# Kernel tuning notes

Hardware: AMD Instinct MI355X
Metric: run time of the kernel (lower is better)

The kernel has to match this reference:

```python
import jax, jax.numpy as jnp
import numpy as np

B, T, C, H = 4, 2048, 1024, 16
DK = C // H


def setup_inputs() -> dict:
    key = jax.random.key(0)
    ks = jax.random.split(key, 12)
    s = 1.0 / np.sqrt(C)
    return {
        "q": jax.random.normal(ks[0], (B, T, C), jnp.float32),
        "k": jax.random.normal(ks[1], (B, T, C), jnp.float32),
        "v": jax.random.normal(ks[2], (B, T, C), jnp.float32),
        "mask": jax.random.randint(ks[3], (B, T, T), 0, 2, jnp.int32),
        "Wq": jax.random.normal(ks[4], (C, C), jnp.float32) * s,
        "bq": jnp.zeros((C,), jnp.float32),
        "Wk": jax.random.normal(ks[5], (C, C), jnp.float32) * s,
        "bk": jnp.zeros((C,), jnp.float32),
        "Wv": jax.random.normal(ks[6], (C, C), jnp.float32) * s,
        "bv": jnp.zeros((C,), jnp.float32),
        "Wf": jax.random.normal(ks[7], (C, C), jnp.float32) * s,
        "bf": jnp.zeros((C,), jnp.float32),
    }


def reference(q, k, v, mask, Wq, bq, Wk, bk, Wv, bv, Wf, bf):
    # linear projections (torch Linear: x @ W.T + b), then split heads
    def heads(x, W, b):
        y = x @ W.T + b  # [B,T,C]
        return y.reshape(B, T, H, DK).transpose(0, 2, 1, 3)  # [B,H,T,DK]

    qh, kh, vh = heads(q, Wq, bq), heads(k, Wk, bk), heads(v, Wv, bv)
    att = jnp.einsum("bhqd,bhkd->bhqk", qh, kh) * (1.0 / np.sqrt(DK))
    att = jnp.where(mask[:, None, :, :] == 0, jnp.float32(-1e9), att)
    p = jax.nn.softmax(att, axis=-1)
    y = jnp.einsum("bhqk,bhkd->bhqd", p, vh)  # [B,H,T,DK]
    y = y.transpose(0, 2, 1, 3).reshape(B, T, C)
    return y @ Wf.T + bf
```

## Files before the change

### kernel.cpp

```cpp
#include <hip/hip_runtime.h>

#define B_ 4
#define T_ 2048
#define C_ 1024
#define H_ 16
#define DK_ 64
#define BT_ 8192

using u16 = unsigned short;
using u32 = unsigned int;
using u64 = unsigned long long;
typedef __attribute__((ext_vector_type(8))) short short8;
typedef __attribute__((ext_vector_type(4))) float f32x4;
typedef __attribute__((ext_vector_type(16))) float f32x16;
typedef __attribute__((ext_vector_type(4))) u32 u32x4;
typedef __attribute__((ext_vector_type(2))) u32 u32x2;

__device__ __forceinline__ u16 f2bf(float f) {
  u32 u = __builtin_bit_cast(u32, f);
  u32 r = u + 0x7fffu + ((u >> 16) & 1u);
  return (u16)(r >> 16);
}

__device__ __forceinline__ void glds16(void* lds, const void* g) {
  __builtin_amdgcn_global_load_lds(
      (__attribute__((address_space(1))) u32*)g,
      (__attribute__((address_space(3))) u32*)lds, 16, 0, 0);
}

__device__ __forceinline__ u32 cvtpk_bf16(float lo, float hi) {
  u32 r;
  asm("v_cvt_pk_bf16_f32 %0, %1, %2" : "=v"(r) : "v"(lo), "v"(hi));
  return r;
}

__device__ __forceinline__ void cvt_range(const float* __restrict__ s,
                                          u16* __restrict__ d, int n,
                                          int rb, int nblk) {
  int i0 = (rb * 256 + (int)threadIdx.x) * 4;
  int stride = nblk * 256 * 4;
  for (int i = i0; i < n; i += stride) {
    float4 v = *(const float4*)(s + i);
    u64 p = (u64)f2bf(v.x) | ((u64)f2bf(v.y) << 16) |
            ((u64)f2bf(v.z) << 32) | ((u64)f2bf(v.w) << 48);
    *(u64*)(d + i) = p;
  }
}

__global__ __launch_bounds__(256) void prep_k(
    const float* __restrict__ q, const float* __restrict__ k,
    const float* __restrict__ v, const float* __restrict__ Wq,
    const float* __restrict__ Wk, const float* __restrict__ Wv,
    const float* __restrict__ Wf,
    u16* __restrict__ qb, u16* __restrict__ kb, u16* __restrict__ vb,
    u16* __restrict__ Wqb, u16* __restrict__ Wkb, u16* __restrict__ Wvb,
    u16* __restrict__ Wfb) {
  const int bid = blockIdx.x;
  if (bid < 1890) {
    const int which = bid / 630, rb = bid % 630;
    const float* s = which == 0 ? q : which == 1 ? k : v;
    u16* d = which == 0 ? qb : which == 1 ? kb : vb;
    cvt_range(s, d, BT_ * C_, rb, 630);
  } else if (bid < 2046) {
    const int idx = bid - 1890;
    const int which = idx / 39, rb = idx % 39;
    const float* s = which == 0 ? Wq : which == 1 ? Wk : which == 2 ? Wv : Wf;
    u16* d = which == 0 ? Wqb : which == 1 ? Wkb : which == 2 ? Wvb : Wfb;
    cvt_range(s, d, C_ * C_, rb, 39);
  }
}

__global__ __launch_bounds__(256) void proj_k(
    const u16* __restrict__ qb, const u16* __restrict__ kb,
    const u16* __restrict__ vb,
    const u16* __restrict__ Wqb, const u16* __restrict__ Wkb,
    const u16* __restrict__ Wvb,
    const float* __restrict__ bq, const float* __restrict__ bk,
    const float* __restrict__ bv,
    u16* __restrict__ Qh, u16* __restrict__ Kh, u16* __restrict__ Vt,
    const int* __restrict__ mask, u64* __restrict__ mb, float qscale) {
  __shared__ __align__(16) u16 As[128 * 32];
  __shared__ __align__(16) u16 Bs[128 * 32];
  const int z = blockIdx.z;
  const int t = threadIdx.x;

  if (z == 3) {
    const int fid = blockIdx.y * 64 + blockIdx.x;
    const int lane = t & 63;
    const int nch = B_ * T_ * T_ / 256;
    int g0 = fid * 16 + (t >> 6) * 4;
    for (int g = g0; g < nch; g += 512 * 16) {
#pragma unroll
      for (int gg = 0; gg < 4; ++gg) {
        const int4 vv = *(const int4*)(mask + (size_t)(g + gg) * 256 + 4 * lane);
        const u64 b0 = __ballot(vv.x != 0);
        const u64 b1 = __ballot(vv.y != 0);
        const u64 b2 = __ballot(vv.z != 0);
        const u64 b3 = __ballot(vv.w != 0);
        const u64 wv = lane == 0 ? b0 : lane == 1 ? b1 : lane == 2 ? b2 : b3;
        if (lane < 4) mb[(size_t)(g + gg) * 4 + lane] = wv;
      }
    }
    return;
  }

  const u16* A = z == 0 ? qb : z == 1 ? kb : Wvb;
  const u16* Bm = z == 0 ? Wqb : z == 1 ? Wkb : vb;
  const float* bias = z == 0 ? bq : z == 1 ? bk : bv;
  u16* out = z == 0 ? Qh : z == 1 ? Kh : Vt;
  const float scale = z == 0 ? qscale : 1.0f;
  const int m0 = (z == 2 ? blockIdx.y : blockIdx.x) * 128;
  const int n0 = (z == 2 ? blockIdx.x : blockIdx.y) * 128;
  const int N = z == 2 ? BT_ : C_;
  const int K = C_;

  const int lane = t & 63;
  const int wave = t >> 6;
  const int wr = wave >> 1, wc = wave & 1;
  const int lr = lane & 15, lg = lane >> 4;

  f32x4 acc[4][4] = {};

  const int srow = t >> 2;
  const int scol = (t & 3) * 8;
  const u16* ag = A + (size_t)(m0 + srow) * K + scol;
  const u16* bg = Bm + (size_t)(n0 + srow) * K + scol;
  u16* as0 = &As[srow * 32 + scol];
  u16* as1 = &As[(srow + 64) * 32 + scol];
  u16* bs0 = &Bs[srow * 32 + scol];
  u16* bs1 = &Bs[(srow + 64) * 32 + scol];

  for (int k0 = 0; k0 < K; k0 += 32) {
    glds16(as0, ag + k0);
    glds16(as1, ag + (size_t)64 * K + k0);
    glds16(bs0, bg + k0);
    glds16(bs1, bg + (size_t)64 * K + k0);
    __syncthreads();
    short8 af[4], bf[4];
#pragma unroll
    for (int m = 0; m < 4; ++m)
      af[m] = *(const short8*)&As[(wr * 64 + m * 16 + lr) * 32 + lg * 8];
#pragma unroll
    for (int n = 0; n < 4; ++n)
      bf[n] = *(const short8*)&Bs[(wc * 64 + n * 16 + lr) * 32 + lg * 8];
#pragma unroll
    for (int m = 0; m < 4; ++m)
#pragma unroll
      for (int n = 0; n < 4; ++n)
        acc[m][n] = __builtin_amdgcn_mfma_f32_16x16x32_bf16(af[m], bf[n], acc[m][n], 0, 0, 0);
    __syncthreads();
  }

#pragma unroll
  for (int m = 0; m < 4; ++m) {
#pragma unroll
    for (int n = 0; n < 4; ++n) {
#pragma unroll
      for (int j = 0; j < 4; ++j) {
        const int gm = m0 + wr * 64 + m * 16 + lg * 4 + j;
        const int gn = n0 + wc * 64 + n * 16 + lr;
        float v = acc[m][n][j];
        if (z <= 1) {
          v = (v + bias[gn]) * scale;
          const int b = gm >> 11, tt = gm & 2047, h = gn >> 6, d = gn & 63;
          out[((((size_t)b * H_ + h) * T_ + tt) << 6) + d] = f2bf(v);
        } else {
          v += bias[gm];
          const int gnp = (gn & ~12) | ((gn & 4) << 1) | ((gn & 8) >> 1);
          out[(size_t)gm * N + gnp] = f2bf(v);
        }
      }
    }
  }
}

__global__ __launch_bounds__(256) void out_k(
    const u16* __restrict__ A, const u16* __restrict__ Bm,
    const float* __restrict__ bias, float* __restrict__ out,
    int M, int N, int K) {
  __shared__ __align__(16) u16 As[128 * 32];
  __shared__ __align__(16) u16 Bs[128 * 32];
  const int t = threadIdx.x;
  const int lane = t & 63;
  const int wave = t >> 6;
  const int wr = wave >> 1, wc = wave & 1;
  const int lr = lane & 15, lg = lane >> 4;
  const int m0 = blockIdx.x * 128;
  const int n0 = blockIdx.y * 128;

  f32x4 acc[4][4] = {};

  const int srow = t >> 2;
  const int scol = (t & 3) * 8;
  const u16* ag = A + (size_t)(m0 + srow) * K + scol;
  const u16* bg = Bm + (size_t)(n0 + srow) * K + scol;
  u16* as0 = &As[srow * 32 + scol];
  u16* as1 = &As[(srow + 64) * 32 + scol];
  u16* bs0 = &Bs[srow * 32 + scol];
  u16* bs1 = &Bs[(srow + 64) * 32 + scol];

  for (int k0 = 0; k0 < K; k0 += 32) {
    glds16(as0, ag + k0);
    glds16(as1, ag + (size_t)64 * K + k0);
    glds16(bs0, bg + k0);
    glds16(bs1, bg + (size_t)64 * K + k0);
    __syncthreads();
    short8 af[4], bf[4];
#pragma unroll
    for (int m = 0; m < 4; ++m)
      af[m] = *(const short8*)&As[(wr * 64 + m * 16 + lr) * 32 + lg * 8];
#pragma unroll
    for (int n = 0; n < 4; ++n)
      bf[n] = *(const short8*)&Bs[(wc * 64 + n * 16 + lr) * 32 + lg * 8];
#pragma unroll
    for (int m = 0; m < 4; ++m)
#pragma unroll
      for (int n = 0; n < 4; ++n)
        acc[m][n] = __builtin_amdgcn_mfma_f32_16x16x32_bf16(af[m], bf[n], acc[m][n], 0, 0, 0);
    __syncthreads();
  }

#pragma unroll
  for (int m = 0; m < 4; ++m)
#pragma unroll
    for (int n = 0; n < 4; ++n)
#pragma unroll
      for (int j = 0; j < 4; ++j) {
        const int gm = m0 + wr * 64 + m * 16 + lg * 4 + j;
        const int gn = n0 + wc * 64 + n * 16 + lr;
        out[(size_t)gm * N + gn] = acc[m][n][j] + bias[gn];
      }
}

__global__ __launch_bounds__(512) void attn32_k(
    const u16* __restrict__ Qh, const u16* __restrict__ Kh,
    const u16* __restrict__ Vt, const u64* __restrict__ mb,
    u16* __restrict__ Y) {
  __shared__ __align__(16) u16 Ks[2][128 * 68];
  __shared__ __align__(16) u16 Vs[2][64 * 132];

  const int f = blockIdx.x;
  const int lgid = ((f & 7) << 6) | (f >> 3);
  const int bh = lgid >> 3, qblk = lgid & 7;
  const int b = bh >> 4, h = bh & 15;
  const int t = threadIdx.x;
  const int wave = t >> 6, lane = t & 63;
  const int lq = lane & 31, hi = lane >> 5;
  const int q0 = qblk * 256 + wave * 32;

  const u16* Qp = Qh + ((size_t)bh * T_ + q0 + lq) * DK_ + hi * 8;
  short8 qf[4];
#pragma unroll
  for (int kt = 0; kt < 4; ++kt) qf[kt] = *(const short8*)(Qp + kt * 16);

  const u16* KgB = Kh + (size_t)bh * T_ * DK_;
  const u16* VtB = Vt + (size_t)h * DK_ * BT_ + (size_t)b * T_;
  const u64* mrow = mb + ((size_t)b * T_ + q0 + lq) * (T_ / 64);

  const int kr = t >> 3, ku = t & 7;
  const u16* ksrcA = KgB + (size_t)kr * DK_ + ku * 8;
  const u16* ksrcB = KgB + (size_t)(kr + 64) * DK_ + ku * 8;
  const int kdstA = kr * 68 + ku * 8, kdstB = (kr + 64) * 68 + ku * 8;
  const int vr = t >> 4, vu = t & 15;
  const u16* vsrcA = VtB + (size_t)vr * BT_ + vu * 8;
  const u16* vsrcB = VtB + (size_t)(vr + 32) * BT_ + vu * 8;
  const int vdstA = vr * 132 + vu * 8, vdstB = (vr + 32) * 132 + vu * 8;

  const u32x4 onesu = {0x3F803F80u, 0x3F803F80u, 0x3F803F80u, 0x3F803F80u};
  const short8 ones8 = __builtin_bit_cast(short8, onesu);

  f32x16 o0 = {}, o1 = {}, accl = {};

  u32x4 kpA = *(const u32x4*)(ksrcA), kpB = *(const u32x4*)(ksrcB);
  u32x4 vpA = *(const u32x4*)(vsrcA), vpB = *(const u32x4*)(vsrcB);
  *(u32x2*)&Ks[0][kdstA] = (u32x2){kpA[0], kpA[1]};
  *(u32x2*)&Ks[0][kdstA + 4] = (u32x2){kpA[2], kpA[3]};
  *(u32x2*)&Ks[0][kdstB] = (u32x2){kpB[0], kpB[1]};
  *(u32x2*)&Ks[0][kdstB + 4] = (u32x2){kpB[2], kpB[3]};
  *(u32x2*)&Vs[0][vdstA] = (u32x2){vpA[0], vpA[1]};
  *(u32x2*)&Vs[0][vdstA + 4] = (u32x2){vpA[2], vpA[3]};
  *(u32x2*)&Vs[0][vdstB] = (u32x2){vpB[0], vpB[1]};
  *(u32x2*)&Vs[0][vdstB + 4] = (u32x2){vpB[2], vpB[3]};
  __syncthreads();
  int cur = 0;

  for (int kv = 0; kv < T_; kv += 128) {
    const bool pre = (kv + 128) < T_;
    if (pre) {
      kpA = *(const u32x4*)(ksrcA + (size_t)(kv + 128) * DK_);
      kpB = *(const u32x4*)(ksrcB + (size_t)(kv + 128) * DK_);
      vpA = *(const u32x4*)(vsrcA + (kv + 128));
      vpB = *(const u32x4*)(vsrcB + (kv + 128));
    }

#pragma unroll
    for (int s2 = 0; s2 < 2; ++s2) {
      const int kvs = kv + 64 * s2;
      f32x16 c0 = {}, c1 = {};
      __builtin_amdgcn_s_setprio(1);
#pragma unroll
      for (int kt = 0; kt < 4; ++kt) {
        const int ix = (2 * kt + hi) * 8;
        const u32x2 a0 = *(const u32x2*)&Ks[cur][(64 * s2 + lq) * 68 + ix];
        const u32x2 a1 = *(const u32x2*)&Ks[cur][(64 * s2 + lq) * 68 + ix + 4];
        const u32x2 b0 = *(const u32x2*)&Ks[cur][(64 * s2 + lq + 32) * 68 + ix];
        const u32x2 b1 = *(const u32x2*)&Ks[cur][(64 * s2 + lq + 32) * 68 + ix + 4];
        const u32x4 k0u = {a0[0], a0[1], a1[0], a1[1]};
        const u32x4 k1u = {b0[0], b0[1], b1[0], b1[1]};
        c0 = __builtin_amdgcn_mfma_f32_32x32x16_bf16(
            __builtin_bit_cast(short8, k0u), qf[kt], c0, 0, 0, 0);
        c1 = __builtin_amdgcn_mfma_f32_32x32x16_bf16(
            __builtin_bit_cast(short8, k1u), qf[kt], c1, 0, 0, 0);
      }
      __builtin_amdgcn_s_setprio(0);

      const u64* wp = mrow + ((kvs >> 8) << 2);
      const int sh = ((kvs >> 2) & 48) + hi;
      u32 tp[4];
#pragma unroll
      for (int e = 0; e < 4; ++e) tp[e] = (u32)(wp[e] >> sh);
#pragma unroll
      for (int r = 0; r < 16; ++r) {
        const int pp = 2 * (r >> 2);
        const u32 k0m = (u32)(((int)(tp[r & 3] << (31 - pp))) >> 31);
        const u32 k1m = (u32)(((int)(tp[r & 3] << (23 - pp))) >> 31);
        c0[r] = __builtin_bit_cast(
            float, __builtin_bit_cast(u32, __builtin_amdgcn_exp2f(c0[r])) & k0m);
        c1[r] = __builtin_bit_cast(
            float, __builtin_bit_cast(u32, __builtin_amdgcn_exp2f(c1[r])) & k1m);
      }

      u32 pw_[4][4];
#pragma unroll
      for (int g = 0; g < 4; ++g) {
        const int ob = (g & 1) * 8;
#pragma unroll
        for (int w2 = 0; w2 < 4; ++w2) {
          const float lo = (g < 2) ? c0[ob + 2 * w2] : c1[ob + 2 * w2];
          const float hii = (g < 2) ? c0[ob + 2 * w2 + 1] : c1[ob + 2 * w2 + 1];
          pw_[g][w2] = cvtpk_bf16(lo, hii);
        }
      }

      __builtin_amdgcn_s_setprio(1);
#pragma unroll
      for (int g = 0; g < 4; ++g) {
        const int ix = 16 * (4 * s2 + g) + 8 * hi;
        const u32x2 va = *(const u32x2*)&Vs[cur][lq * 132 + ix];
        const u32x2 vb = *(const u32x2*)&Vs[cur][lq * 132 + ix + 4];
        const u32x2 wa = *(const u32x2*)&Vs[cur][(lq + 32) * 132 + ix];
        const u32x2 wb = *(const u32x2*)&Vs[cur][(lq + 32) * 132 + ix + 4];
        const u32x4 pu = {pw_[g][0], pw_[g][1], pw_[g][2], pw_[g][3]};
        const u32x4 v0u = {va[0], va[1], vb[0], vb[1]};
        const u32x4 v1u = {wa[0], wa[1], wb[0], wb[1]};
        const short8 pa = __builtin_bit_cast(short8, pu);
        o0 = __builtin_amdgcn_mfma_f32_32x32x16_bf16(
            pa, __builtin_bit_cast(short8, v0u), o0, 0, 0, 0);
        o1 = __builtin_amdgcn_mfma_f32_32x32x16_bf16(
            pa, __builtin_bit_cast(short8, v1u), o1, 0, 0, 0);
        accl = __builtin_amdgcn_mfma_f32_32x32x16_bf16(pa, ones8, accl, 0, 0, 0);
      }
      __builtin_amdgcn_s_setprio(0);
    }

    if (pre) {
      *(u32x2*)&Ks[cur ^ 1][kdstA] = (u32x2){kpA[0], kpA[1]};
      *(u32x2*)&Ks[cur ^ 1][kdstA + 4] = (u32x2){kpA[2], kpA[3]};
      *(u32x2*)&Ks[cur ^ 1][kdstB] = (u32x2){kpB[0], kpB[1]};
      *(u32x2*)&Ks[cur ^ 1][kdstB + 4] = (u32x2){kpB[2], kpB[3]};
      *(u32x2*)&Vs[cur ^ 1][vdstA] = (u32x2){vpA[0], vpA[1]};
      *(u32x2*)&Vs[cur ^ 1][vdstA + 4] = (u32x2){vpA[2], vpA[3]};
      *(u32x2*)&Vs[cur ^ 1][vdstB] = (u32x2){vpB[0], vpB[1]};
      *(u32x2*)&Vs[cur ^ 1][vdstB + 4] = (u32x2){vpB[2], vpB[3]};
    }
    __syncthreads();
    cur ^= 1;
  }

#pragma unroll
  for (int r = 0; r < 16; ++r) {
    const int row = (r & 3) + 8 * (r >> 2) + 4 * hi;
    const float li = 1.0f / accl[r];
    u16* yp = Y + ((size_t)b * T_ + q0 + row) * C_ + h * DK_ + lq;
    yp[0] = f2bf(o0[r] * li);
    yp[32] = f2bf(o1[r] * li);
  }
}

extern "C" void kernel_launch(void* const* d_in, const int* in_sizes, int n_in,
                              void* d_out, int out_size, void* d_ws, size_t ws_size,
                              hipStream_t stream) {
  const float* q  = (const float*)d_in[0];
  const float* k  = (const float*)d_in[1];
  const float* v  = (const float*)d_in[2];
  const int* mask = (const int*)d_in[3];
  const float* Wq = (const float*)d_in[4];
  const float* bq = (const float*)d_in[5];
  const float* Wk = (const float*)d_in[6];
  const float* bk = (const float*)d_in[7];
  const float* Wv = (const float*)d_in[8];
  const float* bv = (const float*)d_in[9];
  const float* Wf = (const float*)d_in[10];
  const float* bf = (const float*)d_in[11];
  float* out = (float*)d_out;
  char* ws = (char*)d_ws;

  size_t off = 0;
  auto nxt = [&](size_t bytes) -> void* {
    void* p = ws + off;
    off += (bytes + 255) & ~(size_t)255;
    return p;
  };
  const size_t big = (size_t)BT_ * C_ * 2;
  const size_t wsz = (size_t)C_ * C_ * 2;
  u16* qb  = (u16*)nxt(big);
  u16* kb  = (u16*)nxt(big);
  u16* vb  = (u16*)nxt(big);
  u16* Wqb = (u16*)nxt(wsz);
  u16* Wkb = (u16*)nxt(wsz);
  u16* Wvb = (u16*)nxt(wsz);
  u16* Wfb = (u16*)nxt(wsz);
  u16* Qh  = (u16*)nxt(big);
  u16* Kh  = (u16*)nxt(big);
  u16* Vt  = (u16*)nxt(big);
  u16* Yb  = (u16*)nxt(big);
  u64* mb  = (u64*)nxt((size_t)B_ * T_ * (T_ / 64) * 8);

  prep_k<<<2048, 256, 0, stream>>>(q, k, v, Wq, Wk, Wv, Wf,
                                   qb, kb, vb, Wqb, Wkb, Wvb, Wfb);

  const float qscale = 0.125f * 1.4426950408889634f;
  proj_k<<<dim3(64, 8, 4), 256, 0, stream>>>(
      qb, kb, vb, Wqb, Wkb, Wvb, bq, bk, bv, Qh, Kh, Vt, mask, mb, qscale);

  attn32_k<<<B_ * H_ * (T_ / 256), 512, 0, stream>>>(Qh, Kh, Vt, mb, Yb);

  out_k<<<dim3(BT_ / 128, C_ / 128), 256, 0, stream>>>(
      Yb, Wfb, bf, out, BT_, C_, C_);
}
```

Before: 270.5 us.

## Fuse fp32-to-bf16 activation conversion into projection GEMM tile loads

Removes the separate conversion pass for q, k and v. The projection kernel now loads fp32 activation tiles straight into XOR-swizzled LDS and converts them to bf16 when building the MFMA fragments. This avoids writing and re-reading three bf16 copies of the activations, at the cost of doubling LDS tile size and re-reading fp32 tiles across the column blocks. The prep kernel now converts only the weight matrices.

```diff
diff --git a/kernel.cpp b/kernel.cpp
--- a/kernel.cpp
+++ b/kernel.cpp
@@ -48,39 +48,28 @@
 }
 
 __global__ __launch_bounds__(256) void prep_k(
-    const float* __restrict__ q, const float* __restrict__ k,
-    const float* __restrict__ v, const float* __restrict__ Wq,
-    const float* __restrict__ Wk, const float* __restrict__ Wv,
-    const float* __restrict__ Wf,
-    u16* __restrict__ qb, u16* __restrict__ kb, u16* __restrict__ vb,
+    const float* __restrict__ Wq, const float* __restrict__ Wk,
+    const float* __restrict__ Wv, const float* __restrict__ Wf,
     u16* __restrict__ Wqb, u16* __restrict__ Wkb, u16* __restrict__ Wvb,
     u16* __restrict__ Wfb) {
   const int bid = blockIdx.x;
-  if (bid < 1890) {
-    const int which = bid / 630, rb = bid % 630;
-    const float* s = which == 0 ? q : which == 1 ? k : v;
-    u16* d = which == 0 ? qb : which == 1 ? kb : vb;
-    cvt_range(s, d, BT_ * C_, rb, 630);
-  } else if (bid < 2046) {
-    const int idx = bid - 1890;
-    const int which = idx / 39, rb = idx % 39;
-    const float* s = which == 0 ? Wq : which == 1 ? Wk : which == 2 ? Wv : Wf;
-    u16* d = which == 0 ? Wqb : which == 1 ? Wkb : which == 2 ? Wvb : Wfb;
-    cvt_range(s, d, C_ * C_, rb, 39);
-  }
+  const int which = bid >> 7, rb = bid & 127;
+  const float* s = which == 0 ? Wq : which == 1 ? Wk : which == 2 ? Wv : Wf;
+  u16* d = which == 0 ? Wqb : which == 1 ? Wkb : which == 2 ? Wvb : Wfb;
+  cvt_range(s, d, C_ * C_, rb, 128);
 }
 
 __global__ __launch_bounds__(256) void proj_k(
-    const u16* __restrict__ qb, const u16* __restrict__ kb,
-    const u16* __restrict__ vb,
+    const float* __restrict__ qf, const float* __restrict__ kf,
+    const float* __restrict__ vf,
     const u16* __restrict__ Wqb, const u16* __restrict__ Wkb,
     const u16* __restrict__ Wvb,
     const float* __restrict__ bq, const float* __restrict__ bk,
     const float* __restrict__ bv,
     u16* __restrict__ Qh, u16* __restrict__ Kh, u16* __restrict__ Vt,
     const int* __restrict__ mask, u64* __restrict__ mb, float qscale) {
-  __shared__ __align__(16) u16 As[128 * 32];
-  __shared__ __align__(16) u16 Bs[128 * 32];
+  __shared__ __align__(16) u16 As[128 * 64];
+  __shared__ __align__(16) u16 Bs[128 * 64];
   const int z = blockIdx.z;
   const int t = threadIdx.x;
 
@@ -104,8 +93,11 @@
     return;
   }
 
-  const u16* A = z == 0 ? qb : z == 1 ? kb : Wvb;
-  const u16* Bm = z == 0 ? Wqb : z == 1 ? Wkb : vb;
+  const bool afp = (z <= 1);
+  const float* Af = z == 0 ? qf : kf;
+  const u16* Ab = Wvb;
+  const u16* Bb = z == 0 ? Wqb : Wkb;
+  const float* Bf = vf;
   const float* bias = z == 0 ? bq : z == 1 ? bk : bv;
   u16* out = z == 0 ? Qh : z == 1 ? Kh : Vt;
   const float scale = z == 0 ? qscale : 1.0f;
@@ -123,26 +115,62 @@
 
   const int srow = t >> 2;
   const int scol = (t & 3) * 8;
-  const u16* ag = A + (size_t)(m0 + srow) * K + scol;
-  const u16* bg = Bm + (size_t)(n0 + srow) * K + scol;
-  u16* as0 = &As[srow * 32 + scol];
-  u16* as1 = &As[(srow + 64) * 32 + scol];
-  u16* bs0 = &Bs[srow * 32 + scol];
-  u16* bs1 = &Bs[(srow + 64) * 32 + scol];
+  float* Asf = (float*)As;
+  float* Bsf = (float*)Bs;
 
   for (int k0 = 0; k0 < K; k0 += 32) {
-    glds16(as0, ag + k0);
-    glds16(as1, ag + (size_t)64 * K + k0);
-    glds16(bs0, bg + k0);
-    glds16(bs1, bg + (size_t)64 * K + k0);
+    if (afp) {
+#pragma unroll
+      for (int s = 0; s < 4; ++s) {
+        const int c = t + s * 256;
+        const int row = c >> 3, cc = c & 7;
+        glds16(&As[row * 64 + cc * 8],
+               Af + (size_t)(m0 + row) * K + k0 + ((cc ^ (row & 7)) << 2));
+      }
+      glds16(&Bs[srow * 32 + scol], Bb + (size_t)(n0 + srow) * K + k0 + scol);
+      glds16(&Bs[(srow + 64) * 32 + scol],
+             Bb + (size_t)(n0 + srow + 64) * K + k0 + scol);
+    } else {
+      glds16(&As[srow * 32 + scol], Ab + (size_t)(m0 + srow) * K + k0 + scol);
+      glds16(&As[(srow + 64) * 32 + scol],
+             Ab + (size_t)(m0 + srow + 64) * K + k0 + scol);
+#pragma unroll
+      for (int s = 0; s < 4; ++s) {
+        const int c = t + s * 256;
+        const int row = c >> 3, cc = c & 7;
+        glds16(&Bs[row * 64 + cc * 8],
+               Bf + (size_t)(n0 + row) * K + k0 + ((cc ^ (row & 7)) << 2));
+      }
+    }
     __syncthreads();
     short8 af[4], bf[4];
-#pragma unroll
-    for (int m = 0; m < 4; ++m)
-      af[m] = *(const short8*)&As[(wr * 64 + m * 16 + lr) * 32 + lg * 8];
-#pragma unroll
-    for (int n = 0; n < 4; ++n)
-      bf[n] = *(const short8*)&Bs[(wc * 64 + n * 16 + lr) * 32 + lg * 8];
+    if (afp) {
+#pragma unroll
+      for (int m = 0; m < 4; ++m) {
+        const int row = wr * 64 + m * 16 + lr;
+        const f32x4 u0 = *(const f32x4*)&Asf[row * 32 + (((2 * lg) ^ (row & 7)) << 2)];
+        const f32x4 u1 = *(const f32x4*)&Asf[row * 32 + (((2 * lg + 1) ^ (row & 7)) << 2)];
+        const u32x4 p = {cvtpk_bf16(u0[0], u0[1]), cvtpk_bf16(u0[2], u0[3]),
+                         cvtpk_bf16(u1[0], u1[1]), cvtpk_bf16(u1[2], u1[3])};
+        af[m] = __builtin_bit_cast(short8, p);
+      }
+#pragma unroll
+      for (int n = 0; n < 4; ++n)
+        bf[n] = *(const short8*)&Bs[(wc * 64 + n * 16 + lr) * 32 + lg * 8];
+    } else {
+#pragma unroll
+      for (int m = 0; m < 4; ++m)
+        af[m] = *(const short8*)&As[(wr * 64 + m * 16 + lr) * 32 + lg * 8];
+#pragma unroll
+      for (int n = 0; n < 4; ++n) {
+        const int row = wc * 64 + n * 16 + lr;
+        const f32x4 u0 = *(const f32x4*)&Bsf[row * 32 + (((2 * lg) ^ (row & 7)) << 2)];
+        const f32x4 u1 = *(const f32x4*)&Bsf[row * 32 + (((2 * lg + 1) ^ (row & 7)) << 2)];
+        const u32x4 p = {cvtpk_bf16(u0[0], u0[1]), cvtpk_bf16(u0[2], u0[3]),
+                         cvtpk_bf16(u1[0], u1[1]), cvtpk_bf16(u1[2], u1[3])};
+        bf[n] = __builtin_bit_cast(short8, p);
+      }
+    }
 #pragma unroll
     for (int m = 0; m < 4; ++m)
 #pragma unroll
@@ -413,9 +441,6 @@
   };
   const size_t big = (size_t)BT_ * C_ * 2;
   const size_t wsz = (size_t)C_ * C_ * 2;
-  u16* qb  = (u16*)nxt(big);
-  u16* kb  = (u16*)nxt(big);
-  u16* vb  = (u16*)nxt(big);
   u16* Wqb = (u16*)nxt(wsz);
   u16* Wkb = (u16*)nxt(wsz);
   u16* Wvb = (u16*)nxt(wsz);
@@ -426,12 +451,11 @@
   u16* Yb  = (u16*)nxt(big);
   u64* mb  = (u64*)nxt((size_t)B_ * T_ * (T_ / 64) * 8);
 
-  prep_k<<<2048, 256, 0, stream>>>(q, k, v, Wq, Wk, Wv, Wf,
-                                   qb, kb, vb, Wqb, Wkb, Wvb, Wfb);
+  prep_k<<<512, 256, 0, stream>>>(Wq, Wk, Wv, Wf, Wqb, Wkb, Wvb, Wfb);
 
   const float qscale = 0.125f * 1.4426950408889634f;
   proj_k<<<dim3(64, 8, 4), 256, 0, stream>>>(
-      qb, kb, vb, Wqb, Wkb, Wvb, bq, bk, bv, Qh, Kh, Vt, mask, mb, qscale);
+      q, k, v, Wqb, Wkb, Wvb, bq, bk, bv, Qh, Kh, Vt, mask, mb, qscale);
 
   attn32_k<<<B_ * H_ * (T_ / 256), 512, 0, stream>>>(Qh, Kh, Vt, mb, Yb);
 
```

After: 300.1 us. 1.11x slower.

## Give each attention wave 64 query rows and compute softmax denominators with VALU sums

Applied to the files above, without the earlier changes.

The attention kernel now runs 4 waves per block instead of 8, and each wave handles 64 query rows as two 32-row sets. Every K and V fragment read from LDS therefore feeds twice as many MFMAs, which halves LDS traffic per unit of work. The row-sum MFMA against a ones vector is replaced by VALU accumulation of the probabilities, then a cross-lane shuffle reduction before normalisation. The cost is much higher register pressure (four score and four output accumulators per wave), which may lower occupancy or cause spills, and each thread now issues more global loads for the K/V tiles.

```diff
diff --git a/kernel.cpp b/kernel.cpp
--- a/kernel.cpp
+++ b/kernel.cpp
@@ -232,7 +232,7 @@
       }
 }
 
-__global__ __launch_bounds__(512) void attn32_k(
+__global__ __launch_bounds__(256) void attn64_k(
     const u16* __restrict__ Qh, const u16* __restrict__ Kh,
     const u16* __restrict__ Vt, const u64* __restrict__ mb,
     u16* __restrict__ Y) {
@@ -246,57 +246,93 @@
   const int t = threadIdx.x;
   const int wave = t >> 6, lane = t & 63;
   const int lq = lane & 31, hi = lane >> 5;
-  const int q0 = qblk * 256 + wave * 32;
-
-  const u16* Qp = Qh + ((size_t)bh * T_ + q0 + lq) * DK_ + hi * 8;
-  short8 qf[4];
-#pragma unroll
-  for (int kt = 0; kt < 4; ++kt) qf[kt] = *(const short8*)(Qp + kt * 16);
+  const int q0 = qblk * 256 + wave * 64;
+
+  short8 qf0[4], qf1[4];
+  {
+    const u16* Qp0 = Qh + ((size_t)bh * T_ + q0 + lq) * DK_ + hi * 8;
+    const u16* Qp1 = Qp0 + (size_t)32 * DK_;
+#pragma unroll
+    for (int kt = 0; kt < 4; ++kt) {
+      qf0[kt] = *(const short8*)(Qp0 + kt * 16);
+      qf1[kt] = *(const short8*)(Qp1 + kt * 16);
+    }
+  }
 
   const u16* KgB = Kh + (size_t)bh * T_ * DK_;
   const u16* VtB = Vt + (size_t)h * DK_ * BT_ + (size_t)b * T_;
-  const u64* mrow = mb + ((size_t)b * T_ + q0 + lq) * (T_ / 64);
-
-  const int kr = t >> 3, ku = t & 7;
-  const u16* ksrcA = KgB + (size_t)kr * DK_ + ku * 8;
-  const u16* ksrcB = KgB + (size_t)(kr + 64) * DK_ + ku * 8;
-  const int kdstA = kr * 68 + ku * 8, kdstB = (kr + 64) * 68 + ku * 8;
-  const int vr = t >> 4, vu = t & 15;
-  const u16* vsrcA = VtB + (size_t)vr * BT_ + vu * 8;
-  const u16* vsrcB = VtB + (size_t)(vr + 32) * BT_ + vu * 8;
-  const int vdstA = vr * 132 + vu * 8, vdstB = (vr + 32) * 132 + vu * 8;
-
-  const u32x4 onesu = {0x3F803F80u, 0x3F803F80u, 0x3F803F80u, 0x3F803F80u};
-  const short8 ones8 = __builtin_bit_cast(short8, onesu);
-
-  f32x16 o0 = {}, o1 = {}, accl = {};
-
-  u32x4 kpA = *(const u32x4*)(ksrcA), kpB = *(const u32x4*)(ksrcB);
-  u32x4 vpA = *(const u32x4*)(vsrcA), vpB = *(const u32x4*)(vsrcB);
-  *(u32x2*)&Ks[0][kdstA] = (u32x2){kpA[0], kpA[1]};
-  *(u32x2*)&Ks[0][kdstA + 4] = (u32x2){kpA[2], kpA[3]};
-  *(u32x2*)&Ks[0][kdstB] = (u32x2){kpB[0], kpB[1]};
-  *(u32x2*)&Ks[0][kdstB + 4] = (u32x2){kpB[2], kpB[3]};
-  *(u32x2*)&Vs[0][vdstA] = (u32x2){vpA[0], vpA[1]};
-  *(u32x2*)&Vs[0][vdstA + 4] = (u32x2){vpA[2], vpA[3]};
-  *(u32x2*)&Vs[0][vdstB] = (u32x2){vpB[0], vpB[1]};
-  *(u32x2*)&Vs[0][vdstB + 4] = (u32x2){vpB[2], vpB[3]};
+  const u64* mrow0 = mb + ((size_t)b * T_ + q0 + lq) * (T_ / 64);
+  const u64* mrow1 = mrow0 + (size_t)32 * (T_ / 64);
+
+  f32x16 o00 = {}, o01 = {}, o10 = {}, o11 = {};
+  float ps0[4] = {0.f, 0.f, 0.f, 0.f}, ps1[4] = {0.f, 0.f, 0.f, 0.f};
+
+  u32x4 kp[4], vp[4];
+#pragma unroll
+  for (int s = 0; s < 4; ++s) {
+    const int c = t + s * 256;
+    kp[s] = *(const u32x4*)(KgB + (size_t)(c >> 3) * DK_ + (c & 7) * 8);
+    vp[s] = *(const u32x4*)(VtB + (size_t)(c >> 4) * BT_ + (c & 15) * 8);
+  }
+#pragma unroll
+  for (int s = 0; s < 4; ++s) {
+    const int c = t + s * 256;
+    const int kd = (c >> 3) * 68 + (c & 7) * 8;
+    const int vd = (c >> 4) * 132 + (c & 15) * 8;
+    *(u32x2*)&Ks[0][kd] = (u32x2){kp[s][0], kp[s][1]};
+    *(u32x2*)&Ks[0][kd + 4] = (u32x2){kp[s][2], kp[s][3]};
+    *(u32x2*)&Vs[0][vd] = (u32x2){vp[s][0], vp[s][1]};
+    *(u32x2*)&Vs[0][vd + 4] = (u32x2){vp[s][2], vp[s][3]};
+  }
   __syncthreads();
   int cur = 0;
+
+  auto finish_set = [&](f32x16& ca, f32x16& cb, const u64* mrow,
+                        float (&ps)[4], u32 (&pw)[4][4], int kvs) {
+    const u64* wp = mrow + ((kvs >> 8) << 2);
+    const int sh = ((kvs >> 2) & 48) + hi;
+    u32 tp[4];
+#pragma unroll
+    for (int e = 0; e < 4; ++e) tp[e] = (u32)(wp[e] >> sh);
+#pragma unroll
+    for (int r = 0; r < 16; ++r) {
+      const int pp = 2 * (r >> 2);
+      const u32 k0m = (u32)(((int)(tp[r & 3] << (31 - pp))) >> 31);
+      const u32 k1m = (u32)(((int)(tp[r & 3] << (23 - pp))) >> 31);
+      ca[r] = __builtin_bit_cast(
+          float, __builtin_bit_cast(u32, __builtin_amdgcn_exp2f(ca[r])) & k0m);
+      cb[r] = __builtin_bit_cast(
+          float, __builtin_bit_cast(u32, __builtin_amdgcn_exp2f(cb[r])) & k1m);
+      ps[r & 3] += ca[r] + cb[r];
+    }
+#pragma unroll
+    for (int g = 0; g < 4; ++g) {
+      const int ob = (g & 1) * 8;
+#pragma unroll
+      for (int w2 = 0; w2 < 4; ++w2) {
+        const float lo = (g < 2) ? ca[ob + 2 * w2] : cb[ob + 2 * w2];
+        const float hii = (g < 2) ? ca[ob + 2 * w2 + 1] : cb[ob + 2 * w2 + 1];
+        pw[g][w2] = cvtpk_bf16(lo, hii);
+      }
+    }
+  };
 
   for (int kv = 0; kv < T_; kv += 128) {
     const bool pre = (kv + 128) < T_;
     if (pre) {
-      kpA = *(const u32x4*)(ksrcA + (size_t)(kv + 128) * DK_);
-      kpB = *(const u32x4*)(ksrcB + (size_t)(kv + 128) * DK_);
-      vpA = *(const u32x4*)(vsrcA + (kv + 128));
-      vpB = *(const u32x4*)(vsrcB + (kv + 128));
+#pragma unroll
+      for (int s = 0; s < 4; ++s) {
+        const int c = t + s * 256;
+        kp[s] = *(const u32x4*)(KgB + (size_t)(kv + 128 + (c >> 3)) * DK_ + (c & 7) * 8);
+        vp[s] = *(const u32x4*)(VtB + (size_t)(c >> 4) * BT_ + kv + 128 + (c & 15) * 8);
+      }
     }
 
 #pragma unroll
     for (int s2 = 0; s2 < 2; ++s2) {
       const int kvs = kv + 64 * s2;
-      f32x16 c0 = {}, c1 = {};
+
+      f32x16 c00 = {}, c01 = {}, c10 = {}, c11 = {};
       __builtin_amdgcn_s_setprio(1);
 #pragma unroll
       for (int kt = 0; kt < 4; ++kt) {
@@ -307,40 +343,18 @@
         const u32x2 b1 = *(const u32x2*)&Ks[cur][(64 * s2 + lq + 32) * 68 + ix + 4];
         const u32x4 k0u = {a0[0], a0[1], a1[0], a1[1]};
         const u32x4 k1u = {b0[0], b0[1], b1[0], b1[1]};
-        c0 = __builtin_amdgcn_mfma_f32_32x32x16_bf16(
-            __builtin_bit_cast(short8, k0u), qf[kt], c0, 0, 0, 0);
-        c1 = __builtin_amdgcn_mfma_f32_32x32x16_bf16(
-            __builtin_bit_cast(short8, k1u), qf[kt], c1, 0, 0, 0);
+        const short8 k0 = __builtin_bit_cast(short8, k0u);
+        const short8 k1 = __builtin_bit_cast(short8, k1u);
+        c00 = __builtin_amdgcn_mfma_f32_32x32x16_bf16(k0, qf0[kt], c00, 0, 0, 0);
+        c10 = __builtin_amdgcn_mfma_f32_32x32x16_bf16(k0, qf1[kt], c10, 0, 0, 0);
+        c01 = __builtin_amdgcn_mfma_f32_32x32x16_bf16(k1, qf0[kt], c01, 0, 0, 0);
+        c11 = __builtin_amdgcn_mfma_f32_32x32x16_bf16(k1, qf1[kt], c11, 0, 0, 0);
       }
       __builtin_amdgcn_s_setprio(0);
 
-      const u64* wp = mrow + ((kvs >> 8) << 2);
-      const int sh = ((kvs >> 2) & 48) + hi;
-      u32 tp[4];
-#pragma unroll
-      for (int e = 0; e < 4; ++e) tp[e] = (u32)(wp[e] >> sh);
-#pragma unroll
-      for (int r = 0; r < 16; ++r) {
-        const int pp = 2 * (r >> 2);
-        const u32 k0m = (u32)(((int)(tp[r & 3] << (31 - pp))) >> 31);
-        const u32 k1m = (u32)(((int)(tp[r & 3] << (23 - pp))) >> 31);
-        c0[r] = __builtin_bit_cast(
-            float, __builtin_bit_cast(u32, __builtin_amdgcn_exp2f(c0[r])) & k0m);
-        c1[r] = __builtin_bit_cast(
-            float, __builtin_bit_cast(u32, __builtin_amdgcn_exp2f(c1[r])) & k1m);
-      }
-
-      u32 pw_[4][4];
-#pragma unroll
-      for (int g = 0; g < 4; ++g) {
-        const int ob = (g & 1) * 8;
-#pragma unroll
-        for (int w2 = 0; w2 < 4; ++w2) {
-          const float lo = (g < 2) ? c0[ob + 2 * w2] : c1[ob + 2 * w2];
-          const float hii = (g < 2) ? c0[ob + 2 * w2 + 1] : c1[ob + 2 * w2 + 1];
-          pw_[g][w2] = cvtpk_bf16(lo, hii);
-        }
-      }
+      u32 pw0[4][4], pw1[4][4];
+      finish_set(c00, c01, mrow0, ps0, pw0, kvs);
+      finish_set(c10, c11, mrow1, ps1, pw1, kvs);
 
       __builtin_amdgcn_s_setprio(1);
 #pragma unroll
@@ -350,40 +364,54 @@
         const u32x2 vb = *(const u32x2*)&Vs[cur][lq * 132 + ix + 4];
         const u32x2 wa = *(const u32x2*)&Vs[cur][(lq + 32) * 132 + ix];
         const u32x2 wb = *(const u32x2*)&Vs[cur][(lq + 32) * 132 + ix + 4];
-        const u32x4 pu = {pw_[g][0], pw_[g][1], pw_[g][2], pw_[g][3]};
         const u32x4 v0u = {va[0], va[1], vb[0], vb[1]};
         const u32x4 v1u = {wa[0], wa[1], wb[0], wb[1]};
-        const short8 pa = __builtin_bit_cast(short8, pu);
-        o0 = __builtin_amdgcn_mfma_f32_32x32x16_bf16(
-            pa, __builtin_bit_cast(short8, v0u), o0, 0, 0, 0);
-        o1 = __builtin_amdgcn_mfma_f32_32x32x16_bf16(
-            pa, __builtin_bit_cast(short8, v1u), o1, 0, 0, 0);
-        accl = __builtin_amdgcn_mfma_f32_32x32x16_bf16(pa, ones8, accl, 0, 0, 0);
+        const short8 v0 = __builtin_bit_cast(short8, v0u);
+        const short8 v1 = __builtin_bit_cast(short8, v1u);
+        const u32x4 p0u = {pw0[g][0], pw0[g][1], pw0[g][2], pw0[g][3]};
+        const u32x4 p1u = {pw1[g][0], pw1[g][1], pw1[g][2], pw1[g][3]};
+        const short8 pa0 = __builtin_bit_cast(short8, p0u);
+        const short8 pa1 = __builtin_bit_cast(short8, p1u);
+        o00 = __builtin_amdgcn_mfma_f32_32x32x16_bf16(pa0, v0, o00, 0, 0, 0);
+        o01 = __builtin_amdgcn_mfma_f32_32x32x16_bf16(pa0, v1, o01, 0, 0, 0);
+        o10 = __builtin_amdgcn_mfma_f32_32x32x16_bf16(pa1, v0, o10, 0, 0, 0);
+        o11 = __builtin_amdgcn_mfma_f32_32x32x16_bf16(pa1, v1, o11, 0, 0, 0);
       }
       __builtin_amdgcn_s_setprio(0);
     }
 
     if (pre) {
-      *(u32x2*)&Ks[cur ^ 1][kdstA] = (u32x2){kpA[0], kpA[1]};
-      *(u32x2*)&Ks[cur ^ 1][kdstA + 4] = (u32x2){kpA[2], kpA[3]};
-      *(u32x2*)&Ks[cur ^ 1][kdstB] = (u32x2){kpB[0], kpB[1]};
-      *(u32x2*)&Ks[cur ^ 1][kdstB + 4] = (u32x2){kpB[2], kpB[3]};
-      *(u32x2*)&Vs[cur ^ 1][vdstA] = (u32x2){vpA[0], vpA[1]};
-      *(u32x2*)&Vs[cur ^ 1][vdstA + 4] = (u32x2){vpA[2], vpA[3]};
-      *(u32x2*)&Vs[cur ^ 1][vdstB] = (u32x2){vpB[0], vpB[1]};
-      *(u32x2*)&Vs[cur ^ 1][vdstB + 4] = (u32x2){vpB[2], vpB[3]};
+#pragma unroll
+      for (int s = 0; s < 4; ++s) {
+        const int c = t + s * 256;
+        const int kd = (c >> 3) * 68 + (c & 7) * 8;
+        const int vd = (c >> 4) * 132 + (c & 15) * 8;
+        *(u32x2*)&Ks[cur ^ 1][kd] = (u32x2){kp[s][0], kp[s][1]};
+        *(u32x2*)&Ks[cur ^ 1][kd + 4] = (u32x2){kp[s][2], kp[s][3]};
+        *(u32x2*)&Vs[cur ^ 1][vd] = (u32x2){vp[s][0], vp[s][1]};
+        *(u32x2*)&Vs[cur ^ 1][vd + 4] = (u32x2){vp[s][2], vp[s][3]};
+      }
     }
     __syncthreads();
     cur ^= 1;
   }
 
+  const float lp0 = (ps0[0] + ps0[1]) + (ps0[2] + ps0[3]);
+  const float lp1 = (ps1[0] + ps1[1]) + (ps1[2] + ps1[3]);
+  const float linv0 = 1.0f / (lp0 + __shfl_xor(lp0, 32));
+  const float linv1 = 1.0f / (lp1 + __shfl_xor(lp1, 32));
+
 #pragma unroll
   for (int r = 0; r < 16; ++r) {
     const int row = (r & 3) + 8 * (r >> 2) + 4 * hi;
-    const float li = 1.0f / accl[r];
-    u16* yp = Y + ((size_t)b * T_ + q0 + row) * C_ + h * DK_ + lq;
-    yp[0] = f2bf(o0[r] * li);
-    yp[32] = f2bf(o1[r] * li);
+    const float li0 = __shfl(linv0, row);
+    const float li1 = __shfl(linv1, row);
+    u16* yp0 = Y + ((size_t)b * T_ + q0 + row) * C_ + h * DK_ + lq;
+    u16* yp1 = Y + ((size_t)b * T_ + q0 + 32 + row) * C_ + h * DK_ + lq;
+    yp0[0] = f2bf(o00[r] * li0);
+    yp0[32] = f2bf(o01[r] * li0);
+    yp1[0] = f2bf(o10[r] * li1);
+    yp1[32] = f2bf(o11[r] * li1);
   }
 }
 
@@ -433,7 +461,7 @@
   proj_k<<<dim3(64, 8, 4), 256, 0, stream>>>(
       qb, kb, vb, Wqb, Wkb, Wvb, bq, bk, bv, Qh, Kh, Vt, mask, mb, qscale);
 
-  attn32_k<<<B_ * H_ * (T_ / 256), 512, 0, stream>>>(Qh, Kh, Vt, mb, Yb);
+  attn64_k<<<512, 256, 0, stream>>>(Qh, Kh, Vt, mb, Yb);
 
   out_k<<<dim3(BT_ / 128, C_ / 128), 256, 0, stream>>>(
       Yb, Wfb, bf, out, BT_, C_, C_);
```

New measurement: 304.1 us. +12.4%, slower.
